# Performance work log

Measured on AMD Instinct MI355X. Metric: run time of the kernel, lower is better.

Reference implementation:

```python
import jax, jax.numpy as jnp
import numpy as np

N, D, C, S = 100000, 512, 4096, 50000


def setup_inputs() -> dict:
    key = jax.random.key(0)
    k1, k2 = jax.random.split(key)
    X = jax.random.normal(k1, (N, D), dtype=jnp.float32)
    codebook_sum = jax.random.normal(k2, (C, D), dtype=jnp.float32)
    prompt_mask = jnp.arange(N) < S  # first S rows are support (True), rest are queries
    return {"X": X, "codebook_sum": codebook_sum, "prompt_mask": prompt_mask, "num_support": S}


def reference(X, codebook_sum, prompt_mask, num_support):
    # num_support is a static Python int (replaces torch.nonzero(prompt_mask) dynamic split)
    s = num_support
    support = X[:s]                                   # [S, D] support (prompt_mask==True)
    query = X[s:]                                     # [Q, D] queries (prompt_mask==False)
    # dense similarity matmul + top-1 nearest-codebook search + gather
    cos_sim = jnp.einsum('sd,cd->sc', support, codebook_sum)  # [S, C]
    top_idx = jnp.argmax(cos_sim, axis=1)             # [S]
    code_n = codebook_sum[top_idx]                    # [S, D] gathered nearest codes
    # mean-pooled prototypes broadcast over queries
    proto = jnp.mean(support, axis=0)                 # [D]
    proto_code = jnp.mean(code_n, axis=0)             # [D]
    # euclidean distances to each prototype
    query_score = jnp.sqrt(jnp.sum((query - proto) ** 2, axis=1))        # [Q]
    query_score_code = jnp.sqrt(jnp.sum((query - proto_code) ** 2, axis=1))  # [Q]
    return (query_score + query_score_code) / 2
```

## Files before the change

### kernel.cpp

```cpp
#include <hip/hip_runtime.h>
#include <hip/hip_bf16.h>

#define NTOT 100000
#define DIM  512
#define CB   4096
#define SSUP 50000
#define NQ   (NTOT - SSUP)

#define MT2   196
#define MPAD2 (MT2 * 256)
#define NT2   16

typedef __bf16 bf16x8 __attribute__((ext_vector_type(8)));
typedef __bf16 bf16x4 __attribute__((ext_vector_type(4)));
typedef float  f32x4  __attribute__((ext_vector_type(4)));

#define OFF_CBBF   0
#define OFF_XB     4194304
#define OFF_PV     55574528
#define OFF_PI     58785792
#define OFF_PSUM   61997056
#define OFF_PCSUM  61999104
#define OFF_HIST   62001152
#define OFF_TIDX   62017536
#define WS_NEED    (62017536 + 200000)
#define ZERO_BYTES (2048 + 2048 + 16384)

#define F_OFF_PSUM   4194304
#define F_OFF_PCSUM  4196352
#define F_OFF_HIST   4198400
#define F_OFF_TIDX   4214784

__device__ __forceinline__ void load_lds16(const void* g, void* l) {
    __builtin_amdgcn_global_load_lds(
        (const __attribute__((address_space(1))) void*)g,
        (__attribute__((address_space(3))) void*)l, 16, 0, 0);
}

#define BARRIER() __builtin_amdgcn_s_barrier()
#define LGKM0()   do { asm volatile("s_waitcnt lgkmcnt(0)" ::: "memory"); \
                       __builtin_amdgcn_sched_barrier(0); } while (0)
#define VMC(N)    asm volatile("s_waitcnt vmcnt(" #N ")" ::: "memory")

__global__ void k_convert(const float* __restrict__ src, __bf16* __restrict__ dst) {
    int i = (blockIdx.x * 256 + threadIdx.x) * 4;
    float4 v = *(const float4*)(src + i);
    bf16x4 o;
    o[0] = (__bf16)v.x; o[1] = (__bf16)v.y; o[2] = (__bf16)v.z; o[3] = (__bf16)v.w;
    *(bf16x4*)(dst + i) = o;
}

__global__ __launch_bounds__(256)
void k_conv_psum(const float* __restrict__ X, __bf16* __restrict__ Xb,
                 float* __restrict__ protoSum)
{
    __shared__ float red[4][512];
    const int tid  = threadIdx.x;
    const int c8   = (tid & 63) * 8;
    const int rsub = tid >> 6;
    const size_t rbase = (size_t)blockIdx.x * 512 + rsub;

    float acc[8];
    #pragma unroll
    for (int j = 0; j < 8; ++j) acc[j] = 0.f;

    for (int r = 0; r < 512; r += 4) {
        const size_t row = rbase + r;
        const float* p = X + row * DIM + c8;
        float4 v0 = *(const float4*)p;
        float4 v1 = *(const float4*)(p + 4);
        bf16x8 o;
        o[0] = (__bf16)v0.x; o[1] = (__bf16)v0.y; o[2] = (__bf16)v0.z; o[3] = (__bf16)v0.w;
        o[4] = (__bf16)v1.x; o[5] = (__bf16)v1.y; o[6] = (__bf16)v1.z; o[7] = (__bf16)v1.w;
        *(bf16x8*)(Xb + row * DIM + c8) = o;
        if (row < SSUP) {
            acc[0] += v0.x; acc[1] += v0.y; acc[2] += v0.z; acc[3] += v0.w;
            acc[4] += v1.x; acc[5] += v1.y; acc[6] += v1.z; acc[7] += v1.w;
        }
    }
    #pragma unroll
    for (int j = 0; j < 8; ++j) red[rsub][c8 + j] = acc[j];
    __syncthreads();
    if (rsub == 0) {
        #pragma unroll
        for (int j = 0; j < 8; ++j)
            atomicAdd(&protoSum[c8 + j],
                      red[0][c8 + j] + red[1][c8 + j] + red[2][c8 + j] + red[3][c8 + j]);
    }
}


__device__ __forceinline__ void stage_half(const __bf16* __restrict__ g, size_t grow0,
                                           int k0, char* ldsop, int half, int tid)
{
    char* dst = ldsop + half * 16384;
    #pragma unroll
    for (int i = 0; i < 2; ++i) {
        const int ck  = i * 512 + tid;
        const int row = ck >> 3;
        const int sc  = (ck & 7) ^ (row & 7);
        load_lds16(g + (grow0 + (size_t)row) * DIM + k0 + sc * 8, dst + ck * 16);
    }
}

template<int BUFOFF, int MH>
__device__ __forceinline__ void ds_load_A(const char* aptr, int off0, int off1,
                                          bf16x8 (&a)[4][2])
{
    #pragma unroll
    for (int t = 0; t < 4; ++t) {
        const char* p = aptr + BUFOFF + MH * 8192 + t * 2048;
        a[t][0] = *(const bf16x8*)(p + off0);
        a[t][1] = *(const bf16x8*)(p + off1);
    }
}

template<int BUFOFF, int NH>
__device__ __forceinline__ void ds_load_B(const char* bptr, int off0, int off1,
                                          bf16x8 (&b)[2][2])
{
    #pragma unroll
    for (int n = 0; n < 2; ++n) {
        const char* p = bptr + BUFOFF + NH * 4096 + n * 2048;
        b[n][0] = *(const bf16x8*)(p + off0);
        b[n][1] = *(const bf16x8*)(p + off1);
    }
}

template<int MH, int NH>
__device__ __forceinline__ void mfma_quad(const bf16x8 (&a)[4][2], const bf16x8 (&b)[2][2],
                                          f32x4 (&acc)[8][4])
{
    __builtin_amdgcn_s_setprio(1);
    #pragma unroll
    for (int t = 0; t < 4; ++t)
        #pragma unroll
        for (int n = 0; n < 2; ++n)
            #pragma unroll
            for (int ks = 0; ks < 2; ++ks)
                acc[MH * 4 + t][NH * 2 + n] = __builtin_amdgcn_mfma_f32_16x16x32_bf16(
                    a[t][ks], b[n][ks], acc[MH * 4 + t][NH * 2 + n], 0, 0, 0);
    __builtin_amdgcn_s_setprio(0);
    __builtin_amdgcn_sched_barrier(0);
}

__global__ __launch_bounds__(512, 2)
void k_gemm256(const __bf16* __restrict__ Xb, const __bf16* __restrict__ cbb,
               float* __restrict__ pv, int* __restrict__ pi)
{
    __shared__ __align__(16) char lds[131072];

    const int tid  = threadIdx.x;
    const int lane = tid & 63;
    const int wid  = tid >> 6;
    const int wm   = wid >> 2;
    const int wn   = wid & 3;
    const int l15  = lane & 15;
    const int q    = lane >> 4;
    const int nt   = blockIdx.x;
    const int mt   = blockIdx.y;
    const size_t r0  = (size_t)mt * 256;
    const size_t c0g = (size_t)nt * 256;

    const int off0 = l15 * 128 + ((q)     ^ (l15 & 7)) * 16;
    const int off1 = l15 * 128 + ((4 + q) ^ (l15 & 7)) * 16;
    const char* aptr = lds + wm * 16384;
    const char* bptr = lds + wn * 8192;

    f32x4 acc[8][4];
    #pragma unroll
    for (int i = 0; i < 8; ++i)
        #pragma unroll
        for (int j = 0; j < 4; ++j)
            acc[i][j] = (f32x4){0.f, 0.f, 0.f, 0.f};

    bf16x8 a[4][2], b0[2][2], b1[2][2];

    stage_half(Xb,  r0,        0,  lds + 0,     0, tid);
    stage_half(Xb,  r0 + 128,  0,  lds + 0,     1, tid);
    stage_half(cbb, c0g,       0,  lds + 32768, 0, tid);
    stage_half(cbb, c0g + 128, 0,  lds + 32768, 1, tid);
    stage_half(cbb, c0g,       64, lds + 98304, 0, tid);
    stage_half(cbb, c0g + 128, 64, lds + 98304, 1, tid);
    VMC(4);
    BARRIER();

    #pragma unroll 1
    for (int it = 0; it < 3; ++it) {
        const int kA1 = (2 * it + 1) * 64;
        const int k2  = (2 * it + 2) * 64;
        const int kB3 = (2 * it + 3) * 64;
        ds_load_A<0, 0>(aptr, off0, off1, a);
        ds_load_B<32768, 0>(bptr, off0, off1, b0);
        stage_half(Xb, r0, kA1, lds + 65536, 0, tid);
        BARRIER(); LGKM0();
        mfma_quad<0, 0>(a, b0, acc);
        BARRIER();
        ds_load_B<32768, 1>(bptr, off0, off1, b1);
        stage_half(Xb, r0 + 128, kA1, lds + 65536, 1, tid);
        BARRIER(); LGKM0();
        mfma_quad<0, 1>(a, b1, acc);
        BARRIER();
        ds_load_A<0, 1>(aptr, off0, off1, a);
        stage_half(cbb, c0g, k2, lds + 32768, 0, tid);
        BARRIER(); LGKM0();
        mfma_quad<1, 1>(a, b1, acc);
        BARRIER();
        stage_half(cbb, c0g + 128, k2, lds + 32768, 1, tid);
        VMC(4);
        BARRIER();
        mfma_quad<1, 0>(a, b0, acc);
        BARRIER();
        ds_load_A<65536, 0>(aptr, off0, off1, a);
        ds_load_B<98304, 0>(bptr, off0, off1, b0);
        stage_half(Xb, r0, k2, lds + 0, 0, tid);
        BARRIER(); LGKM0();
        mfma_quad<0, 0>(a, b0, acc);
        BARRIER();
        ds_load_B<98304, 1>(bptr, off0, off1, b1);
        stage_half(Xb, r0 + 128, k2, lds + 0, 1, tid);
        BARRIER(); LGKM0();
        mfma_quad<0, 1>(a, b1, acc);
        BARRIER();
        ds_load_A<65536, 1>(aptr, off0, off1, a);
        stage_half(cbb, c0g, kB3, lds + 98304, 0, tid);
        BARRIER(); LGKM0();
        mfma_quad<1, 1>(a, b1, acc);
        BARRIER();
        stage_half(cbb, c0g + 128, kB3, lds + 98304, 1, tid);
        VMC(4);
        BARRIER();
        mfma_quad<1, 0>(a, b0, acc);
        BARRIER();
    }

    {
        const int k7 = 7 * 64;
        ds_load_A<0, 0>(aptr, off0, off1, a);
        ds_load_B<32768, 0>(bptr, off0, off1, b0);
        stage_half(Xb, r0, k7, lds + 65536, 0, tid);
        BARRIER(); LGKM0();
        mfma_quad<0, 0>(a, b0, acc);
        BARRIER();

        ds_load_B<32768, 1>(bptr, off0, off1, b1);
        stage_half(Xb, r0 + 128, k7, lds + 65536, 1, tid);
        BARRIER(); LGKM0();
        mfma_quad<0, 1>(a, b1, acc);
        BARRIER();

        ds_load_A<0, 1>(aptr, off0, off1, a);
        BARRIER(); LGKM0();
        mfma_quad<1, 1>(a, b1, acc);
        BARRIER();

        VMC(0);
        BARRIER();
        mfma_quad<1, 0>(a, b0, acc);
        BARRIER();

        ds_load_A<65536, 0>(aptr, off0, off1, a);
        ds_load_B<98304, 0>(bptr, off0, off1, b0);
        BARRIER(); LGKM0();
        mfma_quad<0, 0>(a, b0, acc);
        BARRIER();

        ds_load_B<98304, 1>(bptr, off0, off1, b1);
        BARRIER(); LGKM0();
        mfma_quad<0, 1>(a, b1, acc);
        BARRIER();

        ds_load_A<65536, 1>(aptr, off0, off1, a);
        BARRIER(); LGKM0();
        mfma_quad<1, 1>(a, b1, acc);
        BARRIER();

        mfma_quad<1, 0>(a, b0, acc);
    }

    float* sv = (float*)lds;
    int*   si = (int*)(lds + 4096);
    #pragma unroll
    for (int fm = 0; fm < 8; ++fm) {
        #pragma unroll
        for (int reg = 0; reg < 4; ++reg) {
            float v = -3.0e38f; int idx = 0;
            #pragma unroll
            for (int fn = 0; fn < 4; ++fn) {
                float x = acc[fm][fn][reg];
                int   c = (int)c0g + wn * 64 + fn * 16 + l15;
                if (x > v) { v = x; idx = c; }
            }
            #pragma unroll
            for (int off = 1; off < 16; off <<= 1) {
                float ov = __shfl_xor(v, off, 64);
                int   oi = __shfl_xor(idx, off, 64);
                if (ov > v) { v = ov; idx = oi; }
            }
            if (l15 == 0) {
                int rl = wm * 128 + fm * 16 + q * 4 + reg;
                sv[rl * 4 + wn] = v;
                si[rl * 4 + wn] = idx;
            }
        }
    }
    __syncthreads();
    if (tid < 256) {
        float v = sv[tid * 4]; int idx = si[tid * 4];
        #pragma unroll
        for (int j = 1; j < 4; ++j) {
            float x = sv[tid * 4 + j];
            if (x > v) { v = x; idx = si[tid * 4 + j]; }
        }
        size_t r = r0 + tid;
        pv[r * 16 + nt] = v;
        pi[r * 16 + nt] = idx;
    }
}

__global__ void k_argmax_reduce16(const float* __restrict__ pv, const int* __restrict__ pi,
                                  int* __restrict__ top_idx) {
    int r = blockIdx.x * 256 + threadIdx.x;
    if (r >= SSUP) return;
    float v = -3.0e38f; int idx = 0;
    #pragma unroll
    for (int j = 0; j < 16; ++j) {
        float x = pv[(size_t)r * 16 + j];
        if (x > v) { v = x; idx = pi[(size_t)r * 16 + j]; }
    }
    top_idx[r] = idx;
}

__global__ void k_proto_sum(const float* __restrict__ X, float* __restrict__ protoSum) {
    const int d = threadIdx.x;
    const int r0 = blockIdx.x * 500;
    float acc = 0.f;
    for (int r = r0; r < r0 + 500; ++r)
        acc += X[(size_t)r * DIM + d];
    atomicAdd(&protoSum[d], acc);
}

__global__ __launch_bounds__(256, 2)
void k_gemm_argmax(const float* __restrict__ X, const __bf16* __restrict__ cbb,
                   int* __restrict__ top_idx)
{
    __shared__ float redv[64][2];
    __shared__ int   redi[64][2];

    const int tid  = threadIdx.x;
    const int wave = tid >> 6;
    const int lane = tid & 63;
    const int wm   = wave >> 1;
    const int wn   = wave & 1;
    const int l15  = lane & 15;
    const int q    = lane >> 4;
    const int r0   = blockIdx.x * 64;

    bf16x8 aflat[2][16];
    #pragma unroll
    for (int tm = 0; tm < 2; ++tm) {
        const int r = r0 + wm * 32 + tm * 16 + l15;
        const bool valid = (r < SSUP);
        const float* xr = X + (size_t)r * DIM + q * 8;
        #pragma unroll
        for (int kt = 0; kt < 16; ++kt) {
            float4 v0, v1;
            if (valid) {
                v0 = *(const float4*)(xr + kt * 32);
                v1 = *(const float4*)(xr + kt * 32 + 4);
            } else {
                v0 = make_float4(0.f, 0.f, 0.f, 0.f);
                v1 = v0;
            }
            bf16x8 f;
            f[0] = (__bf16)v0.x; f[1] = (__bf16)v0.y; f[2] = (__bf16)v0.z; f[3] = (__bf16)v0.w;
            f[4] = (__bf16)v1.x; f[5] = (__bf16)v1.y; f[6] = (__bf16)v1.z; f[7] = (__bf16)v1.w;
            aflat[tm][kt] = f;
        }
    }

    float mx[8];
    int   mi[8];
    #pragma unroll
    for (int i = 0; i < 8; ++i) { mx[i] = -3.0e38f; mi[i] = 0; }
    const f32x4 zero4 = {0.f, 0.f, 0.f, 0.f};

    for (int ct = 0; ct < 32; ++ct) {
        const int c0 = ct * 128 + wn * 64;
        const __bf16* bptr[4];
        #pragma unroll
        for (int tn = 0; tn < 4; ++tn)
            bptr[tn] = cbb + (size_t)(c0 + tn * 16 + l15) * DIM + q * 8;

        f32x4 acc[2][4];
        #pragma unroll
        for (int i = 0; i < 2; ++i)
            #pragma unroll
            for (int j = 0; j < 4; ++j)
                acc[i][j] = zero4;

        #pragma unroll
        for (int kt = 0; kt < 16; ++kt) {
            bf16x8 b[4];
            #pragma unroll
            for (int tn = 0; tn < 4; ++tn)
                b[tn] = *(const bf16x8*)(bptr[tn] + kt * 32);
            #pragma unroll
            for (int tm = 0; tm < 2; ++tm)
                #pragma unroll
                for (int tn = 0; tn < 4; ++tn)
                    acc[tm][tn] = __builtin_amdgcn_mfma_f32_16x16x32_bf16(
                        aflat[tm][kt], b[tn], acc[tm][tn], 0, 0, 0);
        }
        #pragma unroll
        for (int tm = 0; tm < 2; ++tm)
            #pragma unroll
            for (int tn = 0; tn < 4; ++tn)
                #pragma unroll
                for (int reg = 0; reg < 4; ++reg) {
                    float v = acc[tm][tn][reg];
                    int slot = tm * 4 + reg;
                    int col  = c0 + tn * 16 + l15;
                    if (v > mx[slot]) { mx[slot] = v; mi[slot] = col; }
                }
    }

    #pragma unroll
    for (int slot = 0; slot < 8; ++slot) {
        float v  = mx[slot];
        int  idx = mi[slot];
        #pragma unroll
        for (int off = 1; off < 16; off <<= 1) {
            float ov = __shfl_xor(v, off, 64);
            int   oi = __shfl_xor(idx, off, 64);
            if (ov > v) { v = ov; idx = oi; }
        }
        if (l15 == 0) {
            int rowl = wm * 32 + (slot >> 2) * 16 + q * 4 + (slot & 3);
            redv[rowl][wn] = v;
            redi[rowl][wn] = idx;
        }
    }
    __syncthreads();
    if (tid < 64) {
        int r = r0 + tid;
        if (r < SSUP) {
            float v0 = redv[tid][0], v1 = redv[tid][1];
            top_idx[r] = (v1 > v0) ? redi[tid][1] : redi[tid][0];
        }
    }
}

__global__ void k_hist(const int* __restrict__ top_idx, int* __restrict__ hist) {
    __shared__ int lh[CB];
    for (int i = threadIdx.x; i < CB; i += blockDim.x) lh[i] = 0;
    __syncthreads();
    for (int i = blockIdx.x * blockDim.x + threadIdx.x; i < SSUP; i += gridDim.x * blockDim.x)
        atomicAdd(&lh[top_idx[i]], 1);
    __syncthreads();
    for (int i = threadIdx.x; i < CB; i += blockDim.x) {
        int v = lh[i];
        if (v) atomicAdd(&hist[i], v);
    }
}

__global__ void k_proto_code(const float* __restrict__ cb, const int* __restrict__ hist,
                             float* __restrict__ pcSum) {
    const int d  = threadIdx.x;
    const int c0 = blockIdx.x * 64;
    float acc = 0.f;
    for (int c = c0; c < c0 + 64; ++c) {
        float w = (float)hist[c];
        if (w != 0.f) acc += w * cb[(size_t)c * DIM + d];
    }
    atomicAdd(&pcSum[d], acc);
}

__global__ void k_query(const float* __restrict__ X, const float* __restrict__ protoSum,
                        const float* __restrict__ pcSum, float* __restrict__ out) {
    const int lane   = threadIdx.x & 63;
    const int waveId = (blockIdx.x * blockDim.x + threadIdx.x) >> 6;
    const int nwaves = (gridDim.x * blockDim.x) >> 6;
    const float invS = 1.0f / (float)SSUP;

    for (int r = waveId; r < NQ; r += nwaves) {
        const float* xr = X + (size_t)(SSUP + r) * DIM;
        float s1 = 0.f, s2 = 0.f;
        #pragma unroll
        for (int i = 0; i < 2; ++i) {
            int dd = lane * 4 + i * 256;
            float4 xq = *(const float4*)(xr + dd);
            float4 p  = *(const float4*)(protoSum + dd);
            float4 pc = *(const float4*)(pcSum + dd);
            float d0, d1, d2, d3;
            d0 = xq.x - p.x * invS; d1 = xq.y - p.y * invS;
            d2 = xq.z - p.z * invS; d3 = xq.w - p.w * invS;
            s1 += d0 * d0 + d1 * d1 + d2 * d2 + d3 * d3;
            d0 = xq.x - pc.x * invS; d1 = xq.y - pc.y * invS;
            d2 = xq.z - pc.z * invS; d3 = xq.w - pc.w * invS;
            s2 += d0 * d0 + d1 * d1 + d2 * d2 + d3 * d3;
        }
        #pragma unroll
        for (int off = 32; off > 0; off >>= 1) {
            s1 += __shfl_xor(s1, off, 64);
            s2 += __shfl_xor(s2, off, 64);
        }
        if (lane == 0)
            out[r] = 0.5f * (sqrtf(s1) + sqrtf(s2));
    }
}

extern "C" void kernel_launch(void* const* d_in, const int* in_sizes, int n_in,
                              void* d_out, int out_size, void* d_ws, size_t ws_size,
                              hipStream_t stream) {
    const float* X  = (const float*)d_in[0];
    const float* cb = (const float*)d_in[1];
    float* out = (float*)d_out;
    char* ws = (char*)d_ws;

    __bf16* cbb = (__bf16*)(ws + OFF_CBBF);

    if (ws_size >= (size_t)WS_NEED) {
        __bf16* Xb       = (__bf16*)(ws + OFF_XB);
        float*  pv       = (float*)(ws + OFF_PV);
        int*    pi       = (int*)(ws + OFF_PI);
        float*  protoSum = (float*)(ws + OFF_PSUM);
        float*  pcSum    = (float*)(ws + OFF_PCSUM);
        int*    hist     = (int*)(ws + OFF_HIST);
        int*    top_idx  = (int*)(ws + OFF_TIDX);

        hipMemsetAsync(ws + OFF_PSUM, 0, ZERO_BYTES, stream);

        k_convert<<<(CB * DIM) / 1024, 256, 0, stream>>>(cb, cbb);
        k_conv_psum<<<MPAD2 / 512, 256, 0, stream>>>(X, Xb, protoSum);

        dim3 grid(NT2, MT2);
        k_gemm256<<<grid, 512, 0, stream>>>(Xb, cbb, pv, pi);

        k_argmax_reduce16<<<(SSUP + 255) / 256, 256, 0, stream>>>(pv, pi, top_idx);
        k_hist<<<64, 256, 0, stream>>>(top_idx, hist);
        k_proto_code<<<CB / 64, 512, 0, stream>>>(cb, hist, pcSum);
        k_query<<<1024, 256, 0, stream>>>(X, protoSum, pcSum, out);
    } else {
        float*  protoSum = (float*)(ws + F_OFF_PSUM);
        float*  pcSum    = (float*)(ws + F_OFF_PCSUM);
        int*    hist     = (int*)(ws + F_OFF_HIST);
        int*    top_idx  = (int*)(ws + F_OFF_TIDX);

        hipMemsetAsync(ws + F_OFF_PSUM, 0, ZERO_BYTES, stream);

        k_convert<<<(CB * DIM) / 1024, 256, 0, stream>>>(cb, cbb);
        k_proto_sum<<<100, 512, 0, stream>>>(X, protoSum);
        k_gemm_argmax<<<(SSUP + 63) / 64, 256, 0, stream>>>(X, cbb, top_idx);
        k_hist<<<64, 256, 0, stream>>>(top_idx, hist);
        k_proto_code<<<CB / 64, 512, 0, stream>>>(cb, hist, pcSum);
        k_query<<<1024, 256, 0, stream>>>(X, protoSum, pcSum, out);
    }
}
```

Measured before the change: 646.4 us.

## Shrink GEMM tile to 128x128 with swizzled block order and smaller conversion blocks

Replaces the 256x256, 512-thread GEMM-argmax tile with a 128x128, 256-thread tile that uses 64KB of LDS, so 32 column partials per row feed the final argmax reduce. Block indices are remapped in groups of 8 to improve L2 reuse of tiles, and the bf16 conversion kernel now handles 64 rows per block for more parallelism. The smaller tiles give finer wave quantization and higher occupancy, but they reload the operands more often relative to compute and double the partial-result traffic.

```diff
diff --git a/kernel.cpp b/kernel.cpp
--- a/kernel.cpp
+++ b/kernel.cpp
@@ -7,9 +7,11 @@
 #define SSUP 50000
 #define NQ   (NTOT - SSUP)
 
-#define MT2   196
-#define MPAD2 (MT2 * 256)
-#define NT2   16
+#define MTILES 391
+#define MPAD   (MTILES * 128)
+#define NTILES 32
+#define NWG    (MTILES * NTILES)
+#define CPX    (NWG / 8)
 
 typedef __bf16 bf16x8 __attribute__((ext_vector_type(8)));
 typedef __bf16 bf16x4 __attribute__((ext_vector_type(4)));
@@ -17,13 +19,13 @@
 
 #define OFF_CBBF   0
 #define OFF_XB     4194304
-#define OFF_PV     55574528
-#define OFF_PI     58785792
-#define OFF_PSUM   61997056
-#define OFF_PCSUM  61999104
-#define OFF_HIST   62001152
-#define OFF_TIDX   62017536
-#define WS_NEED    (62017536 + 200000)
+#define OFF_PV     55443456
+#define OFF_PI     61849600
+#define OFF_PSUM   68255744
+#define OFF_PCSUM  68257792
+#define OFF_HIST   68259840
+#define OFF_TIDX   68276224
+#define WS_NEED    (68276224 + 200000)
 #define ZERO_BYTES (2048 + 2048 + 16384)
 
 #define F_OFF_PSUM   4194304
@@ -58,13 +60,13 @@
     const int tid  = threadIdx.x;
     const int c8   = (tid & 63) * 8;
     const int rsub = tid >> 6;
-    const size_t rbase = (size_t)blockIdx.x * 512 + rsub;
+    const size_t rbase = (size_t)blockIdx.x * 64 + rsub;
 
     float acc[8];
     #pragma unroll
     for (int j = 0; j < 8; ++j) acc[j] = 0.f;
 
-    for (int r = 0; r < 512; r += 4) {
+    for (int r = 0; r < 64; r += 4) {
         const size_t row = rbase + r;
         const float* p = X + row * DIM + c8;
         float4 v0 = *(const float4*)p;
@@ -93,10 +95,10 @@
 __device__ __forceinline__ void stage_half(const __bf16* __restrict__ g, size_t grow0,
                                            int k0, char* ldsop, int half, int tid)
 {
-    char* dst = ldsop + half * 16384;
+    char* dst = ldsop + half * 8192;
     #pragma unroll
     for (int i = 0; i < 2; ++i) {
-        const int ck  = i * 512 + tid;
+        const int ck  = i * 256 + tid;
         const int row = ck >> 3;
         const int sc  = (ck & 7) ^ (row & 7);
         load_lds16(g + (grow0 + (size_t)row) * DIM + k0 + sc * 8, dst + ck * 16);
@@ -105,11 +107,11 @@
 
 template<int BUFOFF, int MH>
 __device__ __forceinline__ void ds_load_A(const char* aptr, int off0, int off1,
-                                          bf16x8 (&a)[4][2])
-{
-    #pragma unroll
-    for (int t = 0; t < 4; ++t) {
-        const char* p = aptr + BUFOFF + MH * 8192 + t * 2048;
+                                          bf16x8 (&a)[2][2])
+{
+    #pragma unroll
+    for (int t = 0; t < 2; ++t) {
+        const char* p = aptr + BUFOFF + MH * 4096 + t * 2048;
         a[t][0] = *(const bf16x8*)(p + off0);
         a[t][1] = *(const bf16x8*)(p + off1);
     }
@@ -128,60 +130,63 @@
 }
 
 template<int MH, int NH>
-__device__ __forceinline__ void mfma_quad(const bf16x8 (&a)[4][2], const bf16x8 (&b)[2][2],
-                                          f32x4 (&acc)[8][4])
+__device__ __forceinline__ void mfma_quad(const bf16x8 (&a)[2][2], const bf16x8 (&b)[2][2],
+                                          f32x4 (&acc)[4][4])
 {
     __builtin_amdgcn_s_setprio(1);
     #pragma unroll
-    for (int t = 0; t < 4; ++t)
+    for (int t = 0; t < 2; ++t)
         #pragma unroll
         for (int n = 0; n < 2; ++n)
             #pragma unroll
             for (int ks = 0; ks < 2; ++ks)
-                acc[MH * 4 + t][NH * 2 + n] = __builtin_amdgcn_mfma_f32_16x16x32_bf16(
-                    a[t][ks], b[n][ks], acc[MH * 4 + t][NH * 2 + n], 0, 0, 0);
+                acc[MH * 2 + t][NH * 2 + n] = __builtin_amdgcn_mfma_f32_16x16x32_bf16(
+                    a[t][ks], b[n][ks], acc[MH * 2 + t][NH * 2 + n], 0, 0, 0);
     __builtin_amdgcn_s_setprio(0);
     __builtin_amdgcn_sched_barrier(0);
 }
 
-__global__ __launch_bounds__(512, 2)
-void k_gemm256(const __bf16* __restrict__ Xb, const __bf16* __restrict__ cbb,
+__global__ __launch_bounds__(256, 2)
+void k_gemm128(const __bf16* __restrict__ Xb, const __bf16* __restrict__ cbb,
                float* __restrict__ pv, int* __restrict__ pi)
 {
-    __shared__ __align__(16) char lds[131072];
+    __shared__ __align__(16) char lds[65536];
 
     const int tid  = threadIdx.x;
     const int lane = tid & 63;
     const int wid  = tid >> 6;
-    const int wm   = wid >> 2;
-    const int wn   = wid & 3;
+    const int wm   = wid >> 1;
+    const int wn   = wid & 1;
     const int l15  = lane & 15;
     const int q    = lane >> 4;
-    const int nt   = blockIdx.x;
-    const int mt   = blockIdx.y;
-    const size_t r0  = (size_t)mt * 256;
-    const size_t c0g = (size_t)nt * 256;
+
+    const int lin = blockIdx.y * NTILES + blockIdx.x;
+    const int swz = (lin & 7) * CPX + (lin >> 3);
+    const int mt  = swz >> 5;
+    const int nt  = swz & 31;
+    const size_t r0  = (size_t)mt * 128;
+    const size_t c0g = (size_t)nt * 128;
 
     const int off0 = l15 * 128 + ((q)     ^ (l15 & 7)) * 16;
     const int off1 = l15 * 128 + ((4 + q) ^ (l15 & 7)) * 16;
-    const char* aptr = lds + wm * 16384;
-    const char* bptr = lds + wn * 8192;
-
-    f32x4 acc[8][4];
-    #pragma unroll
-    for (int i = 0; i < 8; ++i)
+    const char* aptr = lds + wm * 8192;
+    const char* bptr = lds + 16384 + wn * 8192;
+
+    f32x4 acc[4][4];
+    #pragma unroll
+    for (int i = 0; i < 4; ++i)
         #pragma unroll
         for (int j = 0; j < 4; ++j)
             acc[i][j] = (f32x4){0.f, 0.f, 0.f, 0.f};
 
-    bf16x8 a[4][2], b0[2][2], b1[2][2];
-
-    stage_half(Xb,  r0,        0,  lds + 0,     0, tid);
-    stage_half(Xb,  r0 + 128,  0,  lds + 0,     1, tid);
-    stage_half(cbb, c0g,       0,  lds + 32768, 0, tid);
-    stage_half(cbb, c0g + 128, 0,  lds + 32768, 1, tid);
-    stage_half(cbb, c0g,       64, lds + 98304, 0, tid);
-    stage_half(cbb, c0g + 128, 64, lds + 98304, 1, tid);
+    bf16x8 a[2][2], b0[2][2], b1[2][2];
+
+    stage_half(Xb,  r0,       0,  lds + 0,     0, tid);
+    stage_half(Xb,  r0 + 64,  0,  lds + 0,     1, tid);
+    stage_half(cbb, c0g,      0,  lds + 16384, 0, tid);
+    stage_half(cbb, c0g + 64, 0,  lds + 16384, 1, tid);
+    stage_half(cbb, c0g,      64, lds + 49152, 0, tid);
+    stage_half(cbb, c0g + 64, 64, lds + 49152, 1, tid);
     VMC(4);
     BARRIER();
 
@@ -191,43 +196,43 @@
         const int k2  = (2 * it + 2) * 64;
         const int kB3 = (2 * it + 3) * 64;
         ds_load_A<0, 0>(aptr, off0, off1, a);
+        ds_load_B<0, 0>(bptr, off0, off1, b0);
+        stage_half(Xb, r0, kA1, lds + 32768, 0, tid);
+        BARRIER(); LGKM0();
+        mfma_quad<0, 0>(a, b0, acc);
+        BARRIER();
+        ds_load_B<0, 1>(bptr, off0, off1, b1);
+        stage_half(Xb, r0 + 64, kA1, lds + 32768, 1, tid);
+        BARRIER(); LGKM0();
+        mfma_quad<0, 1>(a, b1, acc);
+        BARRIER();
+        ds_load_A<0, 1>(aptr, off0, off1, a);
+        stage_half(cbb, c0g, k2, lds + 16384, 0, tid);
+        BARRIER(); LGKM0();
+        mfma_quad<1, 1>(a, b1, acc);
+        BARRIER();
+        stage_half(cbb, c0g + 64, k2, lds + 16384, 1, tid);
+        VMC(4);
+        BARRIER();
+        mfma_quad<1, 0>(a, b0, acc);
+        BARRIER();
+        ds_load_A<32768, 0>(aptr, off0, off1, a);
         ds_load_B<32768, 0>(bptr, off0, off1, b0);
-        stage_half(Xb, r0, kA1, lds + 65536, 0, tid);
+        stage_half(Xb, r0, k2, lds + 0, 0, tid);
         BARRIER(); LGKM0();
         mfma_quad<0, 0>(a, b0, acc);
         BARRIER();
         ds_load_B<32768, 1>(bptr, off0, off1, b1);
-        stage_half(Xb, r0 + 128, kA1, lds + 65536, 1, tid);
+        stage_half(Xb, r0 + 64, k2, lds + 0, 1, tid);
         BARRIER(); LGKM0();
         mfma_quad<0, 1>(a, b1, acc);
         BARRIER();
-        ds_load_A<0, 1>(aptr, off0, off1, a);
-        stage_half(cbb, c0g, k2, lds + 32768, 0, tid);
+        ds_load_A<32768, 1>(aptr, off0, off1, a);
+        stage_half(cbb, c0g, kB3, lds + 49152, 0, tid);
         BARRIER(); LGKM0();
         mfma_quad<1, 1>(a, b1, acc);
         BARRIER();
-        stage_half(cbb, c0g + 128, k2, lds + 32768, 1, tid);
-        VMC(4);
-        BARRIER();
-        mfma_quad<1, 0>(a, b0, acc);
-        BARRIER();
-        ds_load_A<65536, 0>(aptr, off0, off1, a);
-        ds_load_B<98304, 0>(bptr, off0, off1, b0);
-        stage_half(Xb, r0, k2, lds + 0, 0, tid);
-        BARRIER(); LGKM0();
-        mfma_quad<0, 0>(a, b0, acc);
-        BARRIER();
-        ds_load_B<98304, 1>(bptr, off0, off1, b1);
-        stage_half(Xb, r0 + 128, k2, lds + 0, 1, tid);
-        BARRIER(); LGKM0();
-        mfma_quad<0, 1>(a, b1, acc);
-        BARRIER();
-        ds_load_A<65536, 1>(aptr, off0, off1, a);
-        stage_half(cbb, c0g, kB3, lds + 98304, 0, tid);
-        BARRIER(); LGKM0();
-        mfma_quad<1, 1>(a, b1, acc);
-        BARRIER();
-        stage_half(cbb, c0g + 128, kB3, lds + 98304, 1, tid);
+        stage_half(cbb, c0g + 64, kB3, lds + 49152, 1, tid);
         VMC(4);
         BARRIER();
         mfma_quad<1, 0>(a, b0, acc);
@@ -237,51 +242,51 @@
     {
         const int k7 = 7 * 64;
         ds_load_A<0, 0>(aptr, off0, off1, a);
+        ds_load_B<0, 0>(bptr, off0, off1, b0);
+        stage_half(Xb, r0, k7, lds + 32768, 0, tid);
+        BARRIER(); LGKM0();
+        mfma_quad<0, 0>(a, b0, acc);
+        BARRIER();
+
+        ds_load_B<0, 1>(bptr, off0, off1, b1);
+        stage_half(Xb, r0 + 64, k7, lds + 32768, 1, tid);
+        BARRIER(); LGKM0();
+        mfma_quad<0, 1>(a, b1, acc);
+        BARRIER();
+
+        ds_load_A<0, 1>(aptr, off0, off1, a);
+        BARRIER(); LGKM0();
+        mfma_quad<1, 1>(a, b1, acc);
+        BARRIER();
+
+        VMC(0);
+        BARRIER();
+        mfma_quad<1, 0>(a, b0, acc);
+        BARRIER();
+
+        ds_load_A<32768, 0>(aptr, off0, off1, a);
         ds_load_B<32768, 0>(bptr, off0, off1, b0);
-        stage_half(Xb, r0, k7, lds + 65536, 0, tid);
         BARRIER(); LGKM0();
         mfma_quad<0, 0>(a, b0, acc);
         BARRIER();
 
         ds_load_B<32768, 1>(bptr, off0, off1, b1);
-        stage_half(Xb, r0 + 128, k7, lds + 65536, 1, tid);
         BARRIER(); LGKM0();
         mfma_quad<0, 1>(a, b1, acc);
         BARRIER();
 
-        ds_load_A<0, 1>(aptr, off0, off1, a);
+        ds_load_A<32768, 1>(aptr, off0, off1, a);
         BARRIER(); LGKM0();
         mfma_quad<1, 1>(a, b1, acc);
         BARRIER();
 
-        VMC(0);
-        BARRIER();
         mfma_quad<1, 0>(a, b0, acc);
-        BARRIER();
-
-        ds_load_A<65536, 0>(aptr, off0, off1, a);
-        ds_load_B<98304, 0>(bptr, off0, off1, b0);
-        BARRIER(); LGKM0();
-        mfma_quad<0, 0>(a, b0, acc);
-        BARRIER();
-
-        ds_load_B<98304, 1>(bptr, off0, off1, b1);
-        BARRIER(); LGKM0();
-        mfma_quad<0, 1>(a, b1, acc);
-        BARRIER();
-
-        ds_load_A<65536, 1>(aptr, off0, off1, a);
-        BARRIER(); LGKM0();
-        mfma_quad<1, 1>(a, b1, acc);
-        BARRIER();
-
-        mfma_quad<1, 0>(a, b0, acc);
-    }
-
-    float* sv = (float*)lds;
-    int*   si = (int*)(lds + 4096);
-    #pragma unroll
-    for (int fm = 0; fm < 8; ++fm) {
+    }
+
+    __shared__ float sv[128][2];
+    __shared__ int   si[128][2];
+    #pragma unroll
+    for (int fm = 0; fm < 4; ++fm) {
         #pragma unroll
         for (int reg = 0; reg < 4; ++reg) {
             float v = -3.0e38f; int idx = 0;
@@ -298,35 +303,30 @@
                 if (ov > v) { v = ov; idx = oi; }
             }
             if (l15 == 0) {
-                int rl = wm * 128 + fm * 16 + q * 4 + reg;
-                sv[rl * 4 + wn] = v;
-                si[rl * 4 + wn] = idx;
+                int rl = wm * 64 + fm * 16 + q * 4 + reg;
+                sv[rl][wn] = v;
+                si[rl][wn] = idx;
             }
         }
     }
     __syncthreads();
-    if (tid < 256) {
-        float v = sv[tid * 4]; int idx = si[tid * 4];
-        #pragma unroll
-        for (int j = 1; j < 4; ++j) {
-            float x = sv[tid * 4 + j];
-            if (x > v) { v = x; idx = si[tid * 4 + j]; }
-        }
+    if (tid < 128) {
+        float v0 = sv[tid][0], v1 = sv[tid][1];
         size_t r = r0 + tid;
-        pv[r * 16 + nt] = v;
-        pi[r * 16 + nt] = idx;
-    }
-}
-
-__global__ void k_argmax_reduce16(const float* __restrict__ pv, const int* __restrict__ pi,
-                                  int* __restrict__ top_idx) {
+        pv[r * 32 + nt] = fmaxf(v0, v1);
+        pi[r * 32 + nt] = (v1 > v0) ? si[tid][1] : si[tid][0];
+    }
+}
+
+__global__ void k_argmax_reduce(const float* __restrict__ pv, const int* __restrict__ pi,
+                                int* __restrict__ top_idx) {
     int r = blockIdx.x * 256 + threadIdx.x;
     if (r >= SSUP) return;
     float v = -3.0e38f; int idx = 0;
-    #pragma unroll
-    for (int j = 0; j < 16; ++j) {
-        float x = pv[(size_t)r * 16 + j];
-        if (x > v) { v = x; idx = pi[(size_t)r * 16 + j]; }
+    #pragma unroll 8
+    for (int j = 0; j < 32; ++j) {
+        float x = pv[(size_t)r * 32 + j];
+        if (x > v) { v = x; idx = pi[(size_t)r * 32 + j]; }
     }
     top_idx[r] = idx;
 }
@@ -532,12 +532,12 @@
         hipMemsetAsync(ws + OFF_PSUM, 0, ZERO_BYTES, stream);
 
         k_convert<<<(CB * DIM) / 1024, 256, 0, stream>>>(cb, cbb);
-        k_conv_psum<<<MPAD2 / 512, 256, 0, stream>>>(X, Xb, protoSum);
-
-        dim3 grid(NT2, MT2);
-        k_gemm256<<<grid, 512, 0, stream>>>(Xb, cbb, pv, pi);
-
-        k_argmax_reduce16<<<(SSUP + 255) / 256, 256, 0, stream>>>(pv, pi, top_idx);
+        k_conv_psum<<<MPAD / 64, 256, 0, stream>>>(X, Xb, protoSum);
+
+        dim3 grid(NTILES, MTILES);
+        k_gemm128<<<grid, 256, 0, stream>>>(Xb, cbb, pv, pi);
+
+        k_argmax_reduce<<<(SSUP + 255) / 256, 256, 0, stream>>>(pv, pi, top_idx);
         k_hist<<<64, 256, 0, stream>>>(top_idx, hist);
         k_proto_code<<<CB / 64, 512, 0, stream>>>(cb, hist, pcSum);
         k_query<<<1024, 256, 0, stream>>>(X, protoSum, pcSum, out);
```

Measured after the change: 754.1 us. 1.17x slower.
